# Kernel optimization log

Hardware: AMD Instinct MI355X
Metric: run time of the kernel (lower is better)

The kernel has to match this reference:

```python
import jax, jax.numpy as jnp
import numpy as np

BSZ, T, H, P, N = 2, 2048, 16, 64, 64

def setup_inputs() -> dict:
    key = jax.random.key(0)
    k1, k2, k3, k4, k5 = jax.random.split(key, 5)
    X = jax.random.normal(k1, (BSZ, T, H, P), dtype=jnp.float32)
    delta = jax.random.uniform(k2, (BSZ, T, H), dtype=jnp.float32)
    Bmat = jax.random.normal(k3, (BSZ, T, N), dtype=jnp.float32)
    Cmat = jax.random.normal(k4, (BSZ, T, N), dtype=jnp.float32)
    # module init: A_log = log(arange(1, n_heads+1))
    A_log = jnp.log(jnp.arange(1, H + 1, dtype=jnp.float32))
    return {"X": X, "delta": delta, "Bmat": Bmat, "Cmat": Cmat, "A_log": A_log}

def reference(X, delta, Bmat, Cmat, A_log):
    # X: [B,T,H,P], delta: [B,T,H], Bmat/Cmat: [B,T,N], A_log: [H]
    Bsz, Tlen, Hh, Pp = X.shape
    Nn = Bmat.shape[-1]
    dA = jnp.exp(delta * -jnp.exp(A_log))  # [B,T,H] per-step scalar decay

    def step(h, inp):
        dA_t, dt_t, X_t, B_t, C_t = inp  # [B,H], [B,H], [B,H,P], [B,N], [B,N]
        # outer-product input: delta * X outer B -> [B,H,P,N]
        dBx = (dt_t[:, :, None, None] * X_t[..., None]) * B_t[:, None, None, :]
        h = dA_t[:, :, None, None] * h + dBx
        y_t = jnp.einsum('bhpn,bn->bhp', h, C_t)
        return h, y_t

    h0 = jnp.zeros((Bsz, Hh, Pp, Nn), dtype=X.dtype)
    xs = (
        jnp.moveaxis(dA, 1, 0),    # [T,B,H]
        jnp.moveaxis(delta, 1, 0), # [T,B,H]
        jnp.moveaxis(X, 1, 0),     # [T,B,H,P]
        jnp.moveaxis(Bmat, 1, 0),  # [T,B,N]
        jnp.moveaxis(Cmat, 1, 0),  # [T,B,N]
    )
    h_last, ys = jax.lax.scan(step, h0, xs)
    y = jnp.moveaxis(ys, 0, 1)  # [B,T,H,P]
    return y, h_last
```

## Files before the change

kernel.cpp:

```cpp
#include <hip/hip_runtime.h>


constexpr int BSZ = 2, T = 2048, H = 16, P = 64, N = 64;
constexpr int L = 64, NC = T / L;
constexpr int LS = 72;
constexpr int FS = 68;

using bf16x8 = __attribute__((ext_vector_type(8))) short;
using f32x4  = __attribute__((ext_vector_type(4))) float;

__device__ inline ushort f2bf(float f) {
    unsigned u = __float_as_uint(f);
    u += 0x7FFFu + ((u >> 16) & 1u);
    return (ushort)(u >> 16);
}
__device__ inline unsigned pack2(float a, float b) {
    return (unsigned)f2bf(a) | ((unsigned)f2bf(b) << 16);
}
__device__ inline float bf2f(ushort h) {
    return __uint_as_float(((unsigned)h) << 16);
}

__global__ __launch_bounds__(256, 3) void p1_intra(
    const float* __restrict__ X, const float* __restrict__ delta,
    const float* __restrict__ Bm, const float* __restrict__ Cm,
    const float* __restrict__ A_log,
    ushort* __restrict__ Ybuf, ushort* __restrict__ Hbuf,
    float* __restrict__ Dchunk)
{
    __shared__ __align__(16) ushort sB [64 * LS];
    __shared__ __align__(16) ushort sC [64 * LS];
    __shared__ __align__(16) ushort sBt[64 * LS];
    __shared__ __align__(16) ushort sXt[64 * LS];
    __shared__ __align__(16) ushort sS [64 * LS];
    __shared__ float sSa[64], sSb[64], sW[64];

    const int tid  = threadIdx.x, lane = tid & 63, w = tid >> 6;
    const int quad = lane >> 4,   l16  = lane & 15;
    const int blk = blockIdx.x;
    const int h   = blk & (H - 1);
    const int c   = (blk >> 4) & (NC - 1);
    const int b   = blk >> 9;
    const int t0  = c * L;
    const int chunkid = (b * H + h) * NC + c;

    {
        const float4* gB4 = (const float4*)(Bm + ((size_t)b * T + t0) * N);
        const float4* gC4 = (const float4*)(Cm + ((size_t)b * T + t0) * N);
        #pragma unroll
        for (int r = 0; r < 4; ++r) {
            int idx = r * 256 + tid, t = idx >> 4, n4 = (idx & 15) << 2;
            float4 vb = gB4[idx], vc = gC4[idx];
            *(uint2*)&sB[t * LS + n4] = make_uint2(pack2(vb.x, vb.y), pack2(vb.z, vb.w));
            *(uint2*)&sC[t * LS + n4] = make_uint2(pack2(vc.x, vc.y), pack2(vc.z, vc.w));
        }
        const float* gB = Bm + ((size_t)b * T + t0) * N;
        #pragma unroll
        for (int i = 0; i < 8; ++i) {
            int tau = (w * 8 + i) * 2;
            *(unsigned*)&sBt[lane * LS + tau] =
                pack2(gB[(size_t)tau * N + lane], gB[(size_t)(tau + 1) * N + lane]);
        }
    }
    {
        const float* gX = X + (((size_t)b * T + t0) * H + h) * P;
        #pragma unroll
        for (int i = 0; i < 8; ++i) {
            int tau = w * 16 + 2 * i;
            *(unsigned*)&sXt[lane * LS + tau] =
                pack2(gX[(size_t)tau * (H * P) + lane],
                      gX[(size_t)(tau + 1) * (H * P) + lane]);
        }
    }
    if (w == 0) {
        float dl = delta[((size_t)b * T + t0 + lane) * H + h];
        float s = -__expf(A_log[h]) * dl;
        #pragma unroll
        for (int off = 1; off < 64; off <<= 1) {
            float u = __shfl_up(s, off, 64);
            if (lane >= off) s += u;
        }
        float sL  = __shfl(s, 63, 64);
        float lnd = __logf(dl);
        sSa[lane] = s;
        sSb[lane] = lnd - s;
        sW [lane] = __expf(sL + lnd - s);
        if (lane == 63) Dchunk[chunkid] = __expf(sL);
    }
    __syncthreads();

    f32x4 g[4];
    #pragma unroll
    for (int j = 0; j < 4; ++j) g[j] = (f32x4){0.f, 0.f, 0.f, 0.f};
    #pragma unroll
    for (int ks = 0; ks < 2; ++ks) {
        const int ko = ks * 32 + quad * 8;
        bf16x8 af = *(const bf16x8*)&sC[(w * 16 + l16) * LS + ko];
        #pragma unroll
        for (int jt = 0; jt < 4; ++jt) {
            bf16x8 bfr = *(const bf16x8*)&sB[(jt * 16 + l16) * LS + ko];
            g[jt] = __builtin_amdgcn_mfma_f32_16x16x32_bf16(af, bfr, g[jt], 0, 0, 0);
        }
    }
    #pragma unroll
    for (int jt = 0; jt < 4; ++jt) {
        const int tau = jt * 16 + l16;
        const float sbv = sSb[tau];
        #pragma unroll
        for (int r = 0; r < 4; ++r) {
            const int t = w * 16 + quad * 4 + r;
            float arg = (tau <= t) ? (sSa[t] + sbv) : -80.0f;
            sS[t * LS + tau] = f2bf(__expf(arg) * g[jt][r]);
        }
    }
    __syncthreads();

    f32x4 ya[4], ha[4];
    #pragma unroll
    for (int j = 0; j < 4; ++j) {
        ya[j] = (f32x4){0.f, 0.f, 0.f, 0.f};
        ha[j] = (f32x4){0.f, 0.f, 0.f, 0.f};
    }
    #pragma unroll
    for (int ks = 0; ks < 2; ++ks) {
        const int ko = ks * 32 + quad * 8;
        bf16x8 sa = *(const bf16x8*)&sS [(w * 16 + l16) * LS + ko];
        bf16x8 xa = *(const bf16x8*)&sXt[(w * 16 + l16) * LS + ko];
        union { bf16x8 v; unsigned u[4]; } xw;
        #pragma unroll
        for (int j2 = 0; j2 < 4; ++j2)
            xw.u[j2] = pack2(bf2f((ushort)xa[2*j2])   * sW[ko + 2*j2],
                             bf2f((ushort)xa[2*j2+1]) * sW[ko + 2*j2+1]);
        #pragma unroll
        for (int jp = 0; jp < 4; ++jp) {
            bf16x8 xb = *(const bf16x8*)&sXt[(jp * 16 + l16) * LS + ko];
            ya[jp] = __builtin_amdgcn_mfma_f32_16x16x32_bf16(sa, xb, ya[jp], 0, 0, 0);
        }
        #pragma unroll
        for (int jn = 0; jn < 4; ++jn) {
            bf16x8 bb = *(const bf16x8*)&sBt[(jn * 16 + l16) * LS + ko];
            ha[jn] = __builtin_amdgcn_mfma_f32_16x16x32_bf16(xw.v, bb, ha[jn], 0, 0, 0);
        }
    }

    __syncthreads();
    #pragma unroll
    for (int jp = 0; jp < 4; ++jp)
        #pragma unroll
        for (int r = 0; r < 4; ++r)
            sS[(w * 16 + quad * 4 + r) * LS + jp * 16 + l16] = f2bf(ya[jp][r]);
    #pragma unroll
    for (int jn = 0; jn < 4; ++jn)
        #pragma unroll
        for (int r = 0; r < 4; ++r)
            sXt[(w * 16 + quad * 4 + r) * LS + jn * 16 + l16] = f2bf(ha[jn][r]);
    __syncthreads();
    ushort* Yt = Ybuf + (size_t)chunkid * 4096;
    ushort* Ht = Hbuf + (size_t)chunkid * 4096;
    #pragma unroll
    for (int i = 0; i < 2; ++i) {
        int j = i * 256 + tid, t = j >> 3, col = (j & 7) * 8;
        *(uint4*)&Yt[j * 8] = *(const uint4*)&sS [t * LS + col];
        *(uint4*)&Ht[j * 8] = *(const uint4*)&sXt[t * LS + col];
    }
}

__global__ __launch_bounds__(256, 4) void p2_scan(
    const float* __restrict__ Dchunk, ushort* __restrict__ Hbuf,
    float* __restrict__ Hlast)
{
    const unsigned gid = blockIdx.x * 256u + threadIdx.x;
    const int bh  = gid >> 11;
    const int rem = gid & 2047;
    unsigned* Hb = (unsigned*)Hbuf;
    unsigned v[NC];
    #pragma unroll
    for (int cc = 0; cc < NC; ++cc)
        v[cc] = Hb[(size_t)(bh * NC + cc) * 2048 + rem];
    float hx = 0.f, hy = 0.f;
    #pragma unroll
    for (int cc = 0; cc < NC; ++cc) {
        const float lo = bf2f((ushort)(v[cc] & 0xffffu));
        const float hi = bf2f((ushort)(v[cc] >> 16));
        v[cc] = pack2(hx, hy);
        const float D = Dchunk[bh * NC + cc];
        hx = D * hx + lo;
        hy = D * hy + hi;
    }
    #pragma unroll
    for (int cc = 0; cc < NC; ++cc)
        Hb[(size_t)(bh * NC + cc) * 2048 + rem] = v[cc];
    ((float2*)Hlast)[gid] = make_float2(hx, hy);
}

__global__ __launch_bounds__(256, 3) void p3_inter(
    const float* __restrict__ delta, const float* __restrict__ Cm,
    const float* __restrict__ A_log, const ushort* __restrict__ Hbuf,
    const ushort* __restrict__ Ybuf, float* __restrict__ Y)
{
    __shared__ __align__(16) ushort sC [64 * LS];
    __shared__ __align__(16) ushort sH [64 * LS];
    __shared__ __align__(16) ushort sYi[64 * LS];
    __shared__ __align__(16) float  sF [64 * FS];
    __shared__ float sLam[64];

    const int tid  = threadIdx.x, lane = tid & 63, w = tid >> 6;
    const int quad = lane >> 4,   l16  = lane & 15;
    const int blk = blockIdx.x;
    const int h   = blk & (H - 1);
    const int c   = (blk >> 4) & (NC - 1);
    const int b   = blk >> 9;
    const int t0  = c * L;
    const int chunkid = (b * H + h) * NC + c;

    {
        const float4* gC4 = (const float4*)(Cm + ((size_t)b * T + t0) * N);
        #pragma unroll
        for (int r = 0; r < 4; ++r) {
            int idx = r * 256 + tid, t = idx >> 4, n4 = (idx & 15) << 2;
            float4 vc = gC4[idx];
            *(uint2*)&sC[t * LS + n4] = make_uint2(pack2(vc.x, vc.y), pack2(vc.z, vc.w));
        }
        const uint4* Hg4 = (const uint4*)(Hbuf + (size_t)chunkid * 4096);
        const uint4* Yg4 = (const uint4*)(Ybuf + (size_t)chunkid * 4096);
        #pragma unroll
        for (int i = 0; i < 2; ++i) {
            int j = i * 256 + tid, t = j >> 3, col = (j & 7) * 8;
            *(uint4*)&sH [t * LS + col] = Hg4[j];
            *(uint4*)&sYi[t * LS + col] = Yg4[j];
        }
    }
    if (w == 0) {
        float dl = delta[((size_t)b * T + t0 + lane) * H + h];
        float s = -__expf(A_log[h]) * dl;
        #pragma unroll
        for (int off = 1; off < 64; off <<= 1) {
            float u = __shfl_up(s, off, 64);
            if (lane >= off) s += u;
        }
        sLam[lane] = __expf(s);
    }
    __syncthreads();

    f32x4 acc[4];
    #pragma unroll
    for (int j = 0; j < 4; ++j) acc[j] = (f32x4){0.f, 0.f, 0.f, 0.f};
    #pragma unroll
    for (int ks = 0; ks < 2; ++ks) {
        const int ko = ks * 32 + quad * 8;
        bf16x8 ca = *(const bf16x8*)&sC[(w * 16 + l16) * LS + ko];
        #pragma unroll
        for (int jp = 0; jp < 4; ++jp) {
            bf16x8 hb = *(const bf16x8*)&sH[(jp * 16 + l16) * LS + ko];
            acc[jp] = __builtin_amdgcn_mfma_f32_16x16x32_bf16(ca, hb, acc[jp], 0, 0, 0);
        }
    }

    #pragma unroll
    for (int jp = 0; jp < 4; ++jp)
        #pragma unroll
        for (int r = 0; r < 4; ++r) {
            const int t = w * 16 + quad * 4 + r;
            const int p = jp * 16 + l16;
            sF[t * FS + p] = bf2f(sYi[t * LS + p]) + sLam[t] * acc[jp][r];
        }
    __syncthreads();

    float* Yg = Y + (((size_t)b * T + t0) * H + h) * P;
    #pragma unroll
    for (int i = 0; i < 4; ++i) {
        int j = i * 256 + tid, t = j >> 4, c4 = j & 15;
        *(float4*)(Yg + (size_t)t * (H * P) + c4 * 4) =
            *(const float4*)&sF[t * FS + c4 * 4];
    }
}

extern "C" void kernel_launch(void* const* d_in, const int* in_sizes, int n_in,
                              void* d_out, int out_size, void* d_ws, size_t ws_size,
                              hipStream_t stream) {
    const float* X     = (const float*)d_in[0];
    const float* delta = (const float*)d_in[1];
    const float* Bm    = (const float*)d_in[2];
    const float* Cm    = (const float*)d_in[3];
    const float* A_log = (const float*)d_in[4];

    float* Y     = (float*)d_out;
    float* Hlast = (float*)d_out + (size_t)BSZ * T * H * P;

    constexpr size_t TILE = 4096;
    constexpr size_t NTILE = (size_t)BSZ * H * NC;
    ushort* Hbuf = (ushort*)d_ws;
    ushort* Ybuf = (ushort*)d_ws + NTILE * TILE;
    float* Dchunk = (float*)((char*)d_ws + 2 * NTILE * TILE * sizeof(ushort));

    const int nblk = BSZ * NC * H;
    p1_intra<<<nblk, 256, 0, stream>>>(X, delta, Bm, Cm, A_log, Ybuf, Hbuf, Dchunk);
    p2_scan<<<(BSZ * H * P * N / 2) / 256, 256, 0, stream>>>(Dchunk, Hbuf, Hlast);
    p3_inter<<<nblk, 256, 0, stream>>>(delta, Cm, A_log, Hbuf, Ybuf, Y);
}
```

Baseline: 100.3 us.

## Move intra-chunk output computation into final kernel, dropping Ybuf round trip

The intra-chunk diagonal output (C·B^T masked by decay, times X) moves from the first kernel into the third. The first kernel then only computes chunk-end states, and the bf16 Ybuf intermediate is no longer written and re-read. The final kernel also writes Y directly from registers rather than staging through an fp32 shared tile, and launch bounds move to 4 blocks per CU. In exchange, k3 rereads B and X, does more work per block, and its direct stores are less coalesced.

```diff
diff --git a/kernel.cpp b/kernel.cpp
--- a/kernel.cpp
+++ b/kernel.cpp
@@ -4,7 +4,6 @@
 constexpr int BSZ = 2, T = 2048, H = 16, P = 64, N = 64;
 constexpr int L = 64, NC = T / L;
 constexpr int LS = 72;
-constexpr int FS = 68;
 
 using bf16x8 = __attribute__((ext_vector_type(8))) short;
 using f32x4  = __attribute__((ext_vector_type(4))) float;
@@ -21,19 +20,14 @@
     return __uint_as_float(((unsigned)h) << 16);
 }
 
-__global__ __launch_bounds__(256, 3) void p1_intra(
+__global__ __launch_bounds__(256, 4) void k1_hend(
     const float* __restrict__ X, const float* __restrict__ delta,
-    const float* __restrict__ Bm, const float* __restrict__ Cm,
-    const float* __restrict__ A_log,
-    ushort* __restrict__ Ybuf, ushort* __restrict__ Hbuf,
-    float* __restrict__ Dchunk)
+    const float* __restrict__ Bm, const float* __restrict__ A_log,
+    ushort* __restrict__ Hbuf, float* __restrict__ Dchunk)
 {
-    __shared__ __align__(16) ushort sB [64 * LS];
-    __shared__ __align__(16) ushort sC [64 * LS];
     __shared__ __align__(16) ushort sBt[64 * LS];
     __shared__ __align__(16) ushort sXt[64 * LS];
-    __shared__ __align__(16) ushort sS [64 * LS];
-    __shared__ float sSa[64], sSb[64], sW[64];
+    __shared__ float sWf[64];
 
     const int tid  = threadIdx.x, lane = tid & 63, w = tid >> 6;
     const int quad = lane >> 4,   l16  = lane & 15;
@@ -45,15 +39,6 @@
     const int chunkid = (b * H + h) * NC + c;
 
     {
-        const float4* gB4 = (const float4*)(Bm + ((size_t)b * T + t0) * N);
-        const float4* gC4 = (const float4*)(Cm + ((size_t)b * T + t0) * N);
-        #pragma unroll
-        for (int r = 0; r < 4; ++r) {
-            int idx = r * 256 + tid, t = idx >> 4, n4 = (idx & 15) << 2;
-            float4 vb = gB4[idx], vc = gC4[idx];
-            *(uint2*)&sB[t * LS + n4] = make_uint2(pack2(vb.x, vb.y), pack2(vb.z, vb.w));
-            *(uint2*)&sC[t * LS + n4] = make_uint2(pack2(vc.x, vc.y), pack2(vc.z, vc.w));
-        }
         const float* gB = Bm + ((size_t)b * T + t0) * N;
         #pragma unroll
         for (int i = 0; i < 8; ++i) {
@@ -80,92 +65,46 @@
             float u = __shfl_up(s, off, 64);
             if (lane >= off) s += u;
         }
-        float sL  = __shfl(s, 63, 64);
-        float lnd = __logf(dl);
-        sSa[lane] = s;
-        sSb[lane] = lnd - s;
-        sW [lane] = __expf(sL + lnd - s);
+        float sL = __shfl(s, 63, 64);
+        sWf[lane] = __expf(sL + __logf(dl) - s);
         if (lane == 63) Dchunk[chunkid] = __expf(sL);
     }
     __syncthreads();
 
-    f32x4 g[4];
-    #pragma unroll
-    for (int j = 0; j < 4; ++j) g[j] = (f32x4){0.f, 0.f, 0.f, 0.f};
-    #pragma unroll
-    for (int ks = 0; ks < 2; ++ks) {
-        const int ko = ks * 32 + quad * 8;
-        bf16x8 af = *(const bf16x8*)&sC[(w * 16 + l16) * LS + ko];
-        #pragma unroll
-        for (int jt = 0; jt < 4; ++jt) {
-            bf16x8 bfr = *(const bf16x8*)&sB[(jt * 16 + l16) * LS + ko];
-            g[jt] = __builtin_amdgcn_mfma_f32_16x16x32_bf16(af, bfr, g[jt], 0, 0, 0);
-        }
-    }
-    #pragma unroll
-    for (int jt = 0; jt < 4; ++jt) {
-        const int tau = jt * 16 + l16;
-        const float sbv = sSb[tau];
-        #pragma unroll
-        for (int r = 0; r < 4; ++r) {
-            const int t = w * 16 + quad * 4 + r;
-            float arg = (tau <= t) ? (sSa[t] + sbv) : -80.0f;
-            sS[t * LS + tau] = f2bf(__expf(arg) * g[jt][r]);
-        }
-    }
-    __syncthreads();
-
-    f32x4 ya[4], ha[4];
-    #pragma unroll
-    for (int j = 0; j < 4; ++j) {
-        ya[j] = (f32x4){0.f, 0.f, 0.f, 0.f};
-        ha[j] = (f32x4){0.f, 0.f, 0.f, 0.f};
-    }
-    #pragma unroll
-    for (int ks = 0; ks < 2; ++ks) {
-        const int ko = ks * 32 + quad * 8;
-        bf16x8 sa = *(const bf16x8*)&sS [(w * 16 + l16) * LS + ko];
+    f32x4 ha[4];
+    #pragma unroll
+    for (int j = 0; j < 4; ++j) ha[j] = (f32x4){0.f, 0.f, 0.f, 0.f};
+    #pragma unroll
+    for (int ks = 0; ks < 2; ++ks) {
+        const int ko = ks * 32 + quad * 8;
         bf16x8 xa = *(const bf16x8*)&sXt[(w * 16 + l16) * LS + ko];
         union { bf16x8 v; unsigned u[4]; } xw;
         #pragma unroll
         for (int j2 = 0; j2 < 4; ++j2)
-            xw.u[j2] = pack2(bf2f((ushort)xa[2*j2])   * sW[ko + 2*j2],
-                             bf2f((ushort)xa[2*j2+1]) * sW[ko + 2*j2+1]);
-        #pragma unroll
-        for (int jp = 0; jp < 4; ++jp) {
-            bf16x8 xb = *(const bf16x8*)&sXt[(jp * 16 + l16) * LS + ko];
-            ya[jp] = __builtin_amdgcn_mfma_f32_16x16x32_bf16(sa, xb, ya[jp], 0, 0, 0);
-        }
+            xw.u[j2] = pack2(bf2f((ushort)xa[2*j2])   * sWf[ko + 2*j2],
+                             bf2f((ushort)xa[2*j2+1]) * sWf[ko + 2*j2+1]);
         #pragma unroll
         for (int jn = 0; jn < 4; ++jn) {
             bf16x8 bb = *(const bf16x8*)&sBt[(jn * 16 + l16) * LS + ko];
             ha[jn] = __builtin_amdgcn_mfma_f32_16x16x32_bf16(xw.v, bb, ha[jn], 0, 0, 0);
         }
     }
-
-    __syncthreads();
-    #pragma unroll
-    for (int jp = 0; jp < 4; ++jp)
+    __syncthreads();
+    #pragma unroll
+    for (int jn = 0; jn < 4; ++jn)
         #pragma unroll
         for (int r = 0; r < 4; ++r)
-            sS[(w * 16 + quad * 4 + r) * LS + jp * 16 + l16] = f2bf(ya[jp][r]);
-    #pragma unroll
-    for (int jn = 0; jn < 4; ++jn)
-        #pragma unroll
-        for (int r = 0; r < 4; ++r)
-            sXt[(w * 16 + quad * 4 + r) * LS + jn * 16 + l16] = f2bf(ha[jn][r]);
-    __syncthreads();
-    ushort* Yt = Ybuf + (size_t)chunkid * 4096;
+            sBt[(w * 16 + quad * 4 + r) * LS + jn * 16 + l16] = f2bf(ha[jn][r]);
+    __syncthreads();
     ushort* Ht = Hbuf + (size_t)chunkid * 4096;
     #pragma unroll
     for (int i = 0; i < 2; ++i) {
         int j = i * 256 + tid, t = j >> 3, col = (j & 7) * 8;
-        *(uint4*)&Yt[j * 8] = *(const uint4*)&sS [t * LS + col];
-        *(uint4*)&Ht[j * 8] = *(const uint4*)&sXt[t * LS + col];
-    }
-}
-
-__global__ __launch_bounds__(256, 4) void p2_scan(
+        *(uint4*)&Ht[j * 8] = *(const uint4*)&sBt[t * LS + col];
+    }
+}
+
+__global__ __launch_bounds__(256, 4) void k2_scan(
     const float* __restrict__ Dchunk, ushort* __restrict__ Hbuf,
     float* __restrict__ Hlast)
 {
@@ -193,16 +132,16 @@
     ((float2*)Hlast)[gid] = make_float2(hx, hy);
 }
 
-__global__ __launch_bounds__(256, 3) void p3_inter(
-    const float* __restrict__ delta, const float* __restrict__ Cm,
+__global__ __launch_bounds__(256, 4) void k3_y(
+    const float* __restrict__ X, const float* __restrict__ delta,
+    const float* __restrict__ Bm, const float* __restrict__ Cm,
     const float* __restrict__ A_log, const ushort* __restrict__ Hbuf,
-    const ushort* __restrict__ Ybuf, float* __restrict__ Y)
+    float* __restrict__ Y)
 {
+    __shared__ __align__(16) ushort sB [64 * LS];
     __shared__ __align__(16) ushort sC [64 * LS];
-    __shared__ __align__(16) ushort sH [64 * LS];
-    __shared__ __align__(16) ushort sYi[64 * LS];
-    __shared__ __align__(16) float  sF [64 * FS];
-    __shared__ float sLam[64];
+    __shared__ __align__(16) ushort sXt[64 * LS];
+    __shared__ float sSa[64], sSb[64], sLam[64];
 
     const int tid  = threadIdx.x, lane = tid & 63, w = tid >> 6;
     const int quad = lane >> 4,   l16  = lane & 15;
@@ -213,21 +152,31 @@
     const int t0  = c * L;
     const int chunkid = (b * H + h) * NC + c;
 
-    {
+    uint4 hreg[2];
+    {
+        const uint4* Hg4 = (const uint4*)(Hbuf + (size_t)chunkid * 4096);
+        hreg[0] = Hg4[tid];
+        hreg[1] = Hg4[256 + tid];
+    }
+    {
+        const float4* gB4 = (const float4*)(Bm + ((size_t)b * T + t0) * N);
         const float4* gC4 = (const float4*)(Cm + ((size_t)b * T + t0) * N);
         #pragma unroll
         for (int r = 0; r < 4; ++r) {
             int idx = r * 256 + tid, t = idx >> 4, n4 = (idx & 15) << 2;
-            float4 vc = gC4[idx];
+            float4 vb = gB4[idx], vc = gC4[idx];
+            *(uint2*)&sB[t * LS + n4] = make_uint2(pack2(vb.x, vb.y), pack2(vb.z, vb.w));
             *(uint2*)&sC[t * LS + n4] = make_uint2(pack2(vc.x, vc.y), pack2(vc.z, vc.w));
         }
-        const uint4* Hg4 = (const uint4*)(Hbuf + (size_t)chunkid * 4096);
-        const uint4* Yg4 = (const uint4*)(Ybuf + (size_t)chunkid * 4096);
-        #pragma unroll
-        for (int i = 0; i < 2; ++i) {
-            int j = i * 256 + tid, t = j >> 3, col = (j & 7) * 8;
-            *(uint4*)&sH [t * LS + col] = Hg4[j];
-            *(uint4*)&sYi[t * LS + col] = Yg4[j];
+    }
+    {
+        const float* gX = X + (((size_t)b * T + t0) * H + h) * P;
+        #pragma unroll
+        for (int i = 0; i < 8; ++i) {
+            int tau = w * 16 + 2 * i;
+            *(unsigned*)&sXt[lane * LS + tau] =
+                pack2(gX[(size_t)tau * (H * P) + lane],
+                      gX[(size_t)(tau + 1) * (H * P) + lane]);
         }
     }
     if (w == 0) {
@@ -238,41 +187,85 @@
             float u = __shfl_up(s, off, 64);
             if (lane >= off) s += u;
         }
+        sSa[lane]  = s;
+        sSb[lane]  = __logf(dl) - s;
         sLam[lane] = __expf(s);
     }
     __syncthreads();
 
-    f32x4 acc[4];
-    #pragma unroll
-    for (int j = 0; j < 4; ++j) acc[j] = (f32x4){0.f, 0.f, 0.f, 0.f};
-    #pragma unroll
-    for (int ks = 0; ks < 2; ++ks) {
-        const int ko = ks * 32 + quad * 8;
-        bf16x8 ca = *(const bf16x8*)&sC[(w * 16 + l16) * LS + ko];
-        #pragma unroll
-        for (int jp = 0; jp < 4; ++jp) {
-            bf16x8 hb = *(const bf16x8*)&sH[(jp * 16 + l16) * LS + ko];
-            acc[jp] = __builtin_amdgcn_mfma_f32_16x16x32_bf16(ca, hb, acc[jp], 0, 0, 0);
-        }
-    }
-
-    #pragma unroll
-    for (int jp = 0; jp < 4; ++jp)
+    f32x4 g[4];
+    #pragma unroll
+    for (int j = 0; j < 4; ++j) g[j] = (f32x4){0.f, 0.f, 0.f, 0.f};
+    #pragma unroll
+    for (int ks = 0; ks < 2; ++ks) {
+        const int ko = ks * 32 + quad * 8;
+        bf16x8 af = *(const bf16x8*)&sC[(w * 16 + l16) * LS + ko];
+        #pragma unroll
+        for (int jt = 0; jt < 4; ++jt) {
+            bf16x8 bfr = *(const bf16x8*)&sB[(jt * 16 + l16) * LS + ko];
+            g[jt] = __builtin_amdgcn_mfma_f32_16x16x32_bf16(af, bfr, g[jt], 0, 0, 0);
+        }
+    }
+    __syncthreads();
+
+    #pragma unroll
+    for (int jt = 0; jt < 4; ++jt) {
+        const int tau = jt * 16 + l16;
+        const float sbv = sSb[tau];
         #pragma unroll
         for (int r = 0; r < 4; ++r) {
             const int t = w * 16 + quad * 4 + r;
-            const int p = jp * 16 + l16;
-            sF[t * FS + p] = bf2f(sYi[t * LS + p]) + sLam[t] * acc[jp][r];
-        }
-    __syncthreads();
+            float arg = (tau <= t) ? (sSa[t] + sbv) : -80.0f;
+            sB[t * LS + tau] = f2bf(__expf(arg) * g[jt][r]);
+        }
+    }
+    __syncthreads();
+
+    f32x4 ya[4];
+    #pragma unroll
+    for (int j = 0; j < 4; ++j) ya[j] = (f32x4){0.f, 0.f, 0.f, 0.f};
+    #pragma unroll
+    for (int ks = 0; ks < 2; ++ks) {
+        const int ko = ks * 32 + quad * 8;
+        bf16x8 sa = *(const bf16x8*)&sB[(w * 16 + l16) * LS + ko];
+        #pragma unroll
+        for (int jp = 0; jp < 4; ++jp) {
+            bf16x8 xb = *(const bf16x8*)&sXt[(jp * 16 + l16) * LS + ko];
+            ya[jp] = __builtin_amdgcn_mfma_f32_16x16x32_bf16(sa, xb, ya[jp], 0, 0, 0);
+        }
+    }
+    __syncthreads();
+
+    #pragma unroll
+    for (int i = 0; i < 2; ++i) {
+        int j = i * 256 + tid, t = j >> 3, col = (j & 7) * 8;
+        *(uint4*)&sXt[t * LS + col] = hreg[i];
+    }
+    __syncthreads();
+
+    f32x4 acc[4];
+    #pragma unroll
+    for (int j = 0; j < 4; ++j) acc[j] = (f32x4){0.f, 0.f, 0.f, 0.f};
+    #pragma unroll
+    for (int ks = 0; ks < 2; ++ks) {
+        const int ko = ks * 32 + quad * 8;
+        bf16x8 ca = *(const bf16x8*)&sC[(w * 16 + l16) * LS + ko];
+        #pragma unroll
+        for (int jp = 0; jp < 4; ++jp) {
+            bf16x8 hb = *(const bf16x8*)&sXt[(jp * 16 + l16) * LS + ko];
+            acc[jp] = __builtin_amdgcn_mfma_f32_16x16x32_bf16(ca, hb, acc[jp], 0, 0, 0);
+        }
+    }
 
     float* Yg = Y + (((size_t)b * T + t0) * H + h) * P;
     #pragma unroll
-    for (int i = 0; i < 4; ++i) {
-        int j = i * 256 + tid, t = j >> 4, c4 = j & 15;
-        *(float4*)(Yg + (size_t)t * (H * P) + c4 * 4) =
-            *(const float4*)&sF[t * FS + c4 * 4];
-    }
+    for (int jp = 0; jp < 4; ++jp)
+        #pragma unroll
+        for (int r = 0; r < 4; ++r) {
+            const int t = w * 16 + quad * 4 + r;
+            Yg[(size_t)t * (H * P) + jp * 16 + l16] =
+                ya[jp][r] + sLam[t] * acc[jp][r];
+        }
 }
 
 extern "C" void kernel_launch(void* const* d_in, const int* in_sizes, int n_in,
@@ -289,12 +282,11 @@
 
     constexpr size_t TILE = 4096;
     constexpr size_t NTILE = (size_t)BSZ * H * NC;
-    ushort* Hbuf = (ushort*)d_ws;
-    ushort* Ybuf = (ushort*)d_ws + NTILE * TILE;
-    float* Dchunk = (float*)((char*)d_ws + 2 * NTILE * TILE * sizeof(ushort));
+    ushort* Hbuf  = (ushort*)d_ws;
+    float* Dchunk = (float*)((char*)d_ws + NTILE * TILE * sizeof(ushort));
 
     const int nblk = BSZ * NC * H;
-    p1_intra<<<nblk, 256, 0, stream>>>(X, delta, Bm, Cm, A_log, Ybuf, Hbuf, Dchunk);
-    p2_scan<<<(BSZ * H * P * N / 2) / 256, 256, 0, stream>>>(Dchunk, Hbuf, Hlast);
-    p3_inter<<<nblk, 256, 0, stream>>>(delta, Cm, A_log, Hbuf, Ybuf, Y);
-}
+    k1_hend<<<nblk, 256, 0, stream>>>(X, delta, Bm, A_log, Hbuf, Dchunk);
+    k2_scan<<<(BSZ * H * P * N / 2) / 256, 256, 0, stream>>>(Dchunk, Hbuf, Hlast);
+    k3_y<<<nblk, 256, 0, stream>>>(X, delta, Bm, Cm, A_log, Hbuf, Y);
+}
```

Measured after the change: 99.55 us. About the same (-0.8%).
